# Kernel optimization log

Hardware: AMD Instinct MI355X
Metric: run time of the kernel (lower is better)

## Reference

```python
import jax, jax.numpy as jnp
import numpy as np


def setup_inputs() -> dict:
    key = jax.random.key(0)
    k1, k2, k3 = jax.random.split(key, 3)
    B, L, D, C = 4, 4096, 1024, 1
    x = jax.random.normal(k1, (B, L, D), dtype=jnp.float32)
    kernel = jax.random.normal(k2, (C, D, L), dtype=jnp.float32)
    Dskip = jax.random.normal(k3, (C, D), dtype=jnp.float32)
    return {"x": x, "kernel": kernel, "D": Dskip}


def reference(x, kernel, D):
    # x: [B, L, H]  kernel: [C, H, L]  D: [C, H]
    L = x.shape[1]
    n = 2 * L
    xt = jnp.transpose(x, (0, 2, 1))  # [B, H, L]
    # soft-threshold the kernel: relu(|k| - 0.1) * sign(k)
    k = jax.nn.relu(jnp.abs(kernel) - 0.1) * jnp.sign(kernel)
    k_f = jnp.fft.rfft(k, n=n)          # [C, H, n//2+1] complex
    x_f = jnp.fft.rfft(xt, n=n)         # [B, H, n//2+1] complex
    y_f = jnp.einsum('bhl,chl->bchl', x_f, k_f)
    y = jnp.fft.irfft(y_f, n=n)[..., :L]            # [B, C, H, L]
    y = y + jnp.einsum('bhl,ch->bchl', xt, D)        # skip term
    # rearrange 'b c h l -> b l (c h)'
    Bn, Cn, Hn, Ln = y.shape
    return jnp.transpose(y, (0, 3, 1, 2)).reshape(Bn, Ln, Cn * Hn)
```

## Files before the change

kernel.cpp:

```cpp
#include <hip/hip_runtime.h>


typedef __attribute__((ext_vector_type(8)))  short s16x8;
typedef __attribute__((ext_vector_type(16))) float f32x16;
typedef __attribute__((ext_vector_type(4)))  float f32x4;
typedef __attribute__((ext_vector_type(4)))  unsigned int u32x4;

constexpr int B_ = 4, L_ = 4096, H_ = 1024;
constexpr int PADX = 256;
constexpr int LX = L_ + PADX;
constexpr int LK = L_ + 32;
constexpr int ST = 256;
constexpr int NST = L_ / ST;

constexpr size_t XT_ELEMS = (size_t)B_ * H_ * LX;
constexpr size_t KR_ELEMS = (size_t)2 * H_ * LK;
constexpr size_t OT_ELEMS = (size_t)B_ * H_ * L_;
constexpr size_t WS_NEEDED = (XT_ELEMS + KR_ELEMS + OT_ELEMS) * sizeof(unsigned short);

constexpr int XS_ROW  = 4320;
constexpr int XS_BLKS = XS_ROW / 8;
constexpr int XS_US   = B_ * XS_ROW;
constexpr int KS_US   = 2 * LK;
constexpr int OAREA_DW = 4 * 132;
constexpr int SMEM_BYTES = XS_US * 2 + KS_US * 2 + 4 * OAREA_DW * 4;

constexpr int nHt = H_ / 64, nLt = L_ / 64;
constexpr int NXB = B_ * nLt * nHt;

__device__ __forceinline__ unsigned short f2bf(float f) {
    unsigned int u = __builtin_bit_cast(unsigned int, f);
    u += 0x7fffu + ((u >> 16) & 1u);
    return (unsigned short)(u >> 16);
}
__device__ __forceinline__ float bf2f(unsigned short u) {
    return __builtin_bit_cast(float, (unsigned int)u << 16);
}

__global__ __launch_bounds__(256)
void prep(const float* __restrict__ x, const float* __restrict__ kin,
          const float* __restrict__ Dk,
          unsigned short* __restrict__ xT, unsigned short* __restrict__ kR)
{
    const int bid = blockIdx.x;
    if (bid < NXB) {
        __shared__ float tile[64][65];
        const int b  = bid / (nLt * nHt);
        const int r0 = bid % (nLt * nHt);
        const int l0 = (r0 / nHt) * 64;
        const int h0 = (r0 % nHt) * 64;
        const int j  = threadIdx.x;
        const int h4 = j & 15;
        const int rg = j >> 4;
        #pragma unroll
        for (int it = 0; it < 4; ++it) {
            const int lr = rg + 16 * it;
            const f32x4 v = *(const f32x4*)(x + ((size_t)b * L_ + l0 + lr) * H_ + h0 + 4 * h4);
            tile[lr][4 * h4 + 0] = v.x; tile[lr][4 * h4 + 1] = v.y;
            tile[lr][4 * h4 + 2] = v.z; tile[lr][4 * h4 + 3] = v.w;
        }
        __syncthreads();
        const int lg = j & 7;
        #pragma unroll
        for (int pp = 0; pp < 2; ++pp) {
            const int hh = (j >> 3) + 32 * pp;
            unsigned int w0 = (unsigned int)f2bf(tile[8*lg+0][hh]) | ((unsigned int)f2bf(tile[8*lg+1][hh]) << 16);
            unsigned int w1 = (unsigned int)f2bf(tile[8*lg+2][hh]) | ((unsigned int)f2bf(tile[8*lg+3][hh]) << 16);
            unsigned int w2 = (unsigned int)f2bf(tile[8*lg+4][hh]) | ((unsigned int)f2bf(tile[8*lg+5][hh]) << 16);
            unsigned int w3 = (unsigned int)f2bf(tile[8*lg+6][hh]) | ((unsigned int)f2bf(tile[8*lg+7][hh]) << 16);
            const u32x4 v = {w0, w1, w2, w3};
            *(u32x4*)(xT + ((size_t)b * H_ + h0 + hh) * LX + PADX + l0 + 8 * lg) = v;
        }
        if (l0 == 0) {
            #pragma unroll
            for (int it = 0; it < 8; ++it) {
                const int idx = j + 256 * it;
                const int row = idx >> 5, off = idx & 31;
                const u32x4 z = {};
                *(u32x4*)(xT + ((size_t)b * H_ + h0 + row) * LX + off * 8) = z;
            }
        }
    } else {
        const int h = bid - NXB;
        const float Dv = Dk[h];
        for (int l = (int)threadIdx.x; l < L_; l += 256) {
            const float a = kin[(size_t)h * L_ + l];
            float v = copysignf(fmaxf(fabsf(a) - 0.1f, 0.0f), a);
            if (l == 0) v += Dv;
            const unsigned short bv = f2bf(v);
            kR[(size_t)h * LK + (L_ - 1 - l)] = bv;
            if (l <= L_ - 2)
                kR[((size_t)H_ + h) * LK + (L_ - 2 - l)] = bv;
        }
        if (threadIdx.x < 32) kR[(size_t)h * LK + L_ + threadIdx.x] = 0;
        if (threadIdx.x < 33) kR[((size_t)H_ + h) * LK + (L_ - 1) + threadIdx.x] = 0;
    }
}

#define BODY(DO0, DO1, DO2, DO3)                                            \
  {                                                                         \
    _Pragma("unroll")                                                       \
    for (int i = 0; i < 16; ++i) {                                          \
      u32x4 aw;                                                             \
      aw.x = abase[8*i+0]; aw.y = abase[8*i+1];                             \
      aw.z = abase[8*i+2]; aw.w = abase[8*i+3];                             \
      const s16x8 af = __builtin_bit_cast(s16x8, aw);                       \
      const int io = 32 * (i >> 1);                                         \
      if (DO3) acc3 = __builtin_amdgcn_mfma_f32_32x32x16_bf16(              \
            af, *(const s16x8*)(((i & 1) ? t3b : t3a) + io), acc3, 0,0,0);  \
      if (DO2) acc2 = __builtin_amdgcn_mfma_f32_32x32x16_bf16(              \
            af, *(const s16x8*)(((i & 1) ? t2b : t2a) + io), acc2, 0,0,0);  \
      if (DO1) acc1 = __builtin_amdgcn_mfma_f32_32x32x16_bf16(              \
            af, *(const s16x8*)(((i & 1) ? t1b : t1a) + io), acc1, 0,0,0);  \
      if (DO0) acc0 = __builtin_amdgcn_mfma_f32_32x32x16_bf16(              \
            af, *(const s16x8*)(((i & 1) ? t0b : t0a) + io), acc0, 0,0,0);  \
    }                                                                       \
    abase -= 128;                                                           \
    if (DO3) { t3a -= 256; t3b -= 256; }                                    \
    if (DO2) { t2a -= 256; t2b -= 256; }                                    \
    if (DO1) { t1a -= 256; t1b -= 256; }                                    \
    if (DO0) { t0a -= 256; t0b -= 256; }                                    \
  }

__global__ __launch_bounds__(256, 2)
void longconv_main(const unsigned short* __restrict__ xT,
                   const unsigned short* __restrict__ kR,
                   unsigned int* __restrict__ outT)
{
    __shared__ __align__(16) unsigned char smem[SMEM_BYTES];
    unsigned short* xs = (unsigned short*)smem;
    unsigned short* ks = (unsigned short*)(smem + (size_t)XS_US * 2);
    float* oarea = (float*)(smem + (size_t)XS_US * 2 + (size_t)KS_US * 2);

    const int h   = blockIdx.x;
    const int tid = threadIdx.x;

    constexpr int NXU = XS_BLKS * 4;
    constexpr int NKU = 2 * (LK / 8);
    for (int u = tid; u < NXU + NKU; u += 256) {
        if (u < NXU) {
            const int b = u / XS_BLKS, n = u - b * XS_BLKS;
            const u32x4 v = *(const u32x4*)(xT + ((size_t)b * H_ + h) * LX + 32 + n * 8);
            *(u32x4*)(xs + (size_t)b * XS_ROW + (size_t)(n ^ b) * 8) = v;
        } else {
            const int v2 = u - NXU;
            const int p = v2 / (LK / 8), i = v2 - p * (LK / 8);
            const u32x4 v = *(const u32x4*)(kR + ((size_t)p * H_ + h) * LK + i * 8);
            *(u32x4*)(ks + (size_t)p * LK + (size_t)i * 8) = v;
        }
    }
    __syncthreads();

    const int w  = tid >> 6, ln = tid & 63;
    const int m  = ln & 31,  q  = ln >> 5;
    const int t  = m >> 2,   b  = m & 3;
    const int si0 = w, si1 = 7 - w, si2 = 8 + w, si3 = 15 - w;

    const int base = 3871 - m + 8 * q;
    const int p    = base & 1;
    const unsigned int* abase = (const unsigned int*)(ks + p * LK + (base - p));
    const unsigned short* xrow = xs + (size_t)b * XS_ROW;
    const int nb = 4 * t + q;

    auto mk = [&](int si, int par) -> const unsigned short* {
        const int n = 32 * si + nb + 2 * par;
        return xrow + (size_t)((n ^ b) * 8);
    };
    const unsigned short *t0a = mk(si0, 0), *t0b = mk(si0, 1);
    const unsigned short *t1a = mk(si1, 0), *t1b = mk(si1, 1);
    const unsigned short *t2a = mk(si2, 0), *t2b = mk(si2, 1);
    const unsigned short *t3a = mk(si3, 0), *t3b = mk(si3, 1);

    f32x16 acc0 = {}, acc1 = {}, acc2 = {}, acc3 = {};
    int beta = 0;
    for (; beta <= si0; ++beta) BODY(1, 1, 1, 1);
    for (; beta <= si1; ++beta) BODY(0, 1, 1, 1);
    for (; beta <= si2; ++beta) BODY(0, 0, 1, 1);
    for (; beta <= si3; ++beta) BODY(0, 0, 0, 1);

    float* ar = oarea + w * OAREA_DW;
    auto writeout = [&](const f32x16& acc, int si) {
        const int Ls = si * ST;
        #pragma unroll
        for (int rh = 0; rh < 2; ++rh) {
            #pragma unroll
            for (int rr2 = 0; rr2 < 2; ++rr2) {
                const int base4 = (8 * rr2 + 4 * q + 4 * t) & 15;
                f32x4 qd;
                qd.x = acc[4 * (2 * rh + rr2) + 0];
                qd.y = acc[4 * (2 * rh + rr2) + 1];
                qd.z = acc[4 * (2 * rh + rr2) + 2];
                qd.w = acc[4 * (2 * rh + rr2) + 3];
                *(f32x4*)(ar + b * 132 + 16 * t + base4) = qd;
            }
            __asm__ volatile("s_waitcnt lgkmcnt(0)" ::: "memory");
            #pragma unroll
            for (int bb = 0; bb < 4; ++bb) {
                const int g  = ln >> 3;
                const int uu = (2 * ln) & 15;
                const int s  = (uu + 4 * g) & 15;
                const float v0 = ar[bb * 132 + 16 * g + s];
                const float v1 = ar[bb * 132 + 16 * g + s + 1];
                const int l = 32 * g + 16 * rh + uu;
                const unsigned int pk =
                    (unsigned int)f2bf(v0) | ((unsigned int)f2bf(v1) << 16);
                outT[(((size_t)bb * H_ + h) * L_ + Ls + l) >> 1] = pk;
            }
            __asm__ volatile("s_waitcnt lgkmcnt(0)" ::: "memory");
        }
    };
    writeout(acc0, si0);
    writeout(acc1, si1);
    writeout(acc2, si2);
    writeout(acc3, si3);
}

__global__ __launch_bounds__(256)
void untranspose(const unsigned short* __restrict__ outT, float* __restrict__ out)
{
    __shared__ float tile[64][65];
    const int bid = blockIdx.x;
    const int b  = bid / (nLt * nHt);
    const int r0 = bid % (nLt * nHt);
    const int l0 = (r0 / nHt) * 64;
    const int h0 = (r0 % nHt) * 64;
    const int j  = threadIdx.x;
    const int lg = j & 7;
    #pragma unroll
    for (int pp = 0; pp < 2; ++pp) {
        const int hh = (j >> 3) + 32 * pp;
        const u32x4 v = *(const u32x4*)(outT + ((size_t)b * H_ + h0 + hh) * L_ + l0 + 8 * lg);
        const unsigned short* pu = (const unsigned short*)&v;
        #pragma unroll
        for (int i = 0; i < 8; ++i) tile[8 * lg + i][hh] = bf2f(pu[i]);
    }
    __syncthreads();
    const int hg = j & 15;
    #pragma unroll
    for (int pp = 0; pp < 4; ++pp) {
        const int ll = (j >> 4) + 16 * pp;
        f32x4 v;
        v.x = tile[ll][4 * hg + 0];
        v.y = tile[ll][4 * hg + 1];
        v.z = tile[ll][4 * hg + 2];
        v.w = tile[ll][4 * hg + 3];
        *(f32x4*)(out + ((size_t)b * L_ + l0 + ll) * H_ + h0 + 4 * hg) = v;
    }
}

constexpr int TLf = 32, Uf = 8, Wf = TLf + Uf - 1, HTf = 256;

__global__ __launch_bounds__(HTf)
void longconv_fp32(const float* __restrict__ x, const float* __restrict__ k,
                   const float* __restrict__ Dskip, float* __restrict__ out)
{
    const int h  = blockIdx.y * HTf + threadIdx.x;
    const int b  = blockIdx.z;
    const int lt = (int)gridDim.x - 1 - (int)blockIdx.x;
    const int L0 = lt * TLf;
    const float* __restrict__ xb = x + ((size_t)b * L_) * H_ + h;
    const float* __restrict__ kh = k + (size_t)h * L_;
    float acc[TLf]; float win[Wf];
    #pragma unroll
    for (int i = 0; i < Wf; ++i) {
        const int idx = L0 - (Uf - 1) + i;
        win[i] = (idx >= 0) ? xb[(size_t)idx * H_] : 0.0f;
    }
    const float Dv = Dskip[h];
    #pragma unroll
    for (int jj = 0; jj < TLf; ++jj) acc[jj] = win[jj + Uf - 1] * Dv;
    const int cmax = L0 / Uf + (TLf / Uf) - 1;
    for (int c = 0; c <= cmax; ++c) {
        float kr[Uf];
        #pragma unroll
        for (int u = 0; u < Uf; ++u) {
            const float a = kh[c * Uf + u];
            kr[u] = copysignf(fmaxf(fabsf(a) - 0.1f, 0.0f), a);
        }
        #pragma unroll
        for (int u = 0; u < Uf; ++u)
            #pragma unroll
            for (int jj = 0; jj < TLf; ++jj)
                acc[jj] = fmaf(kr[u], win[jj + (Uf - 1) - u], acc[jj]);
        if (c < cmax) {
            #pragma unroll
            for (int i = Wf - 1; i >= Uf; --i) win[i] = win[i - Uf];
            #pragma unroll
            for (int i = 0; i < Uf; ++i) {
                const int idx = L0 - (c + 1) * Uf - (Uf - 1) + i;
                win[i] = (idx >= 0) ? xb[(size_t)idx * H_] : 0.0f;
            }
        }
    }
    float* __restrict__ ob = out + ((size_t)b * L_ + L0) * H_ + h;
    #pragma unroll
    for (int jj = 0; jj < TLf; ++jj) ob[(size_t)jj * H_] = acc[jj];
}

extern "C" void kernel_launch(void* const* d_in, const int* in_sizes, int n_in,
                              void* d_out, int out_size, void* d_ws, size_t ws_size,
                              hipStream_t stream)
{
    const float* x  = (const float*)d_in[0];
    const float* k  = (const float*)d_in[1];
    const float* Dk = (const float*)d_in[2];
    float* out = (float*)d_out;

    if (ws_size >= WS_NEEDED) {
        unsigned short* xT = (unsigned short*)d_ws;
        unsigned short* kR = xT + XT_ELEMS;
        unsigned short* oT = kR + KR_ELEMS;
        prep<<<dim3(NXB + H_), dim3(256), 0, stream>>>(x, k, Dk, xT, kR);
        longconv_main<<<dim3(H_), dim3(256), 0, stream>>>(xT, kR, (unsigned int*)oT);
        untranspose<<<dim3(NXB), dim3(256), 0, stream>>>(oT, out);
    } else {
        dim3 grid(L_ / TLf, H_ / HTf, B_);
        longconv_fp32<<<grid, dim3(HTf), 0, stream>>>(x, k, Dk, out);
    }
}
```

Baseline: 215.2 us.

## Pair adjacent output strips and reuse B fragments in registers across beta steps

Each wave now handles two pairs of adjacent 256-sample output strips (2w,2w+1 and 14-2w,15-2w) instead of four scattered strips. The x fragment loaded for the lower strip at step beta is exactly what the higher strip needs at step beta+1. It is kept in a 16-entry register array, which roughly halves LDS reads of B fragments. The cost is 32 extra s16x8 registers per thread, which may cause spills or lower occupancy under launch_bounds(256,2).

Result: no change. 211.6 us (-1.7%).

```diff
diff --git a/kernel.cpp b/kernel.cpp
--- a/kernel.cpp
+++ b/kernel.cpp
@@ -97,29 +97,33 @@
     }
 }
 
-#define BODY(DO0, DO1, DO2, DO3)                                            \
-  {                                                                         \
-    _Pragma("unroll")                                                       \
-    for (int i = 0; i < 16; ++i) {                                          \
-      u32x4 aw;                                                             \
-      aw.x = abase[8*i+0]; aw.y = abase[8*i+1];                             \
-      aw.z = abase[8*i+2]; aw.w = abase[8*i+3];                             \
-      const s16x8 af = __builtin_bit_cast(s16x8, aw);                       \
-      const int io = 32 * (i >> 1);                                         \
-      if (DO3) acc3 = __builtin_amdgcn_mfma_f32_32x32x16_bf16(              \
-            af, *(const s16x8*)(((i & 1) ? t3b : t3a) + io), acc3, 0,0,0);  \
-      if (DO2) acc2 = __builtin_amdgcn_mfma_f32_32x32x16_bf16(              \
-            af, *(const s16x8*)(((i & 1) ? t2b : t2a) + io), acc2, 0,0,0);  \
-      if (DO1) acc1 = __builtin_amdgcn_mfma_f32_32x32x16_bf16(              \
-            af, *(const s16x8*)(((i & 1) ? t1b : t1a) + io), acc1, 0,0,0);  \
-      if (DO0) acc0 = __builtin_amdgcn_mfma_f32_32x32x16_bf16(              \
-            af, *(const s16x8*)(((i & 1) ? t0b : t0a) + io), acc0, 0,0,0);  \
-    }                                                                       \
-    abase -= 128;                                                           \
-    if (DO3) { t3a -= 256; t3b -= 256; }                                    \
-    if (DO2) { t2a -= 256; t2b -= 256; }                                    \
-    if (DO1) { t1a -= 256; t1b -= 256; }                                    \
-    if (DO0) { t0a -= 256; t0b -= 256; }                                    \
+#define BODY2(M1, M2)                                                        \
+  {                                                                          \
+    _Pragma("unroll")                                                        \
+    for (int i = 0; i < 16; ++i) {                                           \
+      u32x4 aw;                                                              \
+      aw.x = abase[8*i+0]; aw.y = abase[8*i+1];                              \
+      aw.z = abase[8*i+2]; aw.w = abase[8*i+3];                              \
+      const s16x8 af = __builtin_bit_cast(s16x8, aw);                        \
+      const int io = 32 * (i >> 1);                                          \
+      if (M2 >= 1) accH2 = __builtin_amdgcn_mfma_f32_32x32x16_bf16(          \
+            af, held2[i], accH2, 0, 0, 0);                                   \
+      if (M2 == 2) {                                                         \
+        const s16x8 nf = *(const s16x8*)(((i & 1) ? p2b : p2a) + io);        \
+        accL2 = __builtin_amdgcn_mfma_f32_32x32x16_bf16(af, nf, accL2,0,0,0);\
+        held2[i] = nf;                                                       \
+      }                                                                      \
+      if (M1 >= 1) accH1 = __builtin_amdgcn_mfma_f32_32x32x16_bf16(          \
+            af, held1[i], accH1, 0, 0, 0);                                   \
+      if (M1 == 2) {                                                         \
+        const s16x8 nf = *(const s16x8*)(((i & 1) ? p1b : p1a) + io);        \
+        accL1 = __builtin_amdgcn_mfma_f32_32x32x16_bf16(af, nf, accL1,0,0,0);\
+        held1[i] = nf;                                                       \
+      }                                                                      \
+    }                                                                        \
+    abase -= 128;                                                            \
+    if (M1 == 2) { p1a -= 256; p1b -= 256; }                                 \
+    if (M2 == 2) { p2a -= 256; p2b -= 256; }                                 \
   }
 
 __global__ __launch_bounds__(256, 2)
@@ -154,7 +158,8 @@
     const int w  = tid >> 6, ln = tid & 63;
     const int m  = ln & 31,  q  = ln >> 5;
     const int t  = m >> 2,   b  = m & 3;
-    const int si0 = w, si1 = 7 - w, si2 = 8 + w, si3 = 15 - w;
+    const int s1 = 2 * w;
+    const int s2 = 14 - 2 * w;
 
     const int base = 3871 - m + 8 * q;
     const int p    = base & 1;
@@ -166,17 +171,24 @@
         const int n = 32 * si + nb + 2 * par;
         return xrow + (size_t)((n ^ b) * 8);
     };
-    const unsigned short *t0a = mk(si0, 0), *t0b = mk(si0, 1);
-    const unsigned short *t1a = mk(si1, 0), *t1b = mk(si1, 1);
-    const unsigned short *t2a = mk(si2, 0), *t2b = mk(si2, 1);
-    const unsigned short *t3a = mk(si3, 0), *t3b = mk(si3, 1);
-
-    f32x16 acc0 = {}, acc1 = {}, acc2 = {}, acc3 = {};
-    int beta = 0;
-    for (; beta <= si0; ++beta) BODY(1, 1, 1, 1);
-    for (; beta <= si1; ++beta) BODY(0, 1, 1, 1);
-    for (; beta <= si2; ++beta) BODY(0, 0, 1, 1);
-    for (; beta <= si3; ++beta) BODY(0, 0, 0, 1);
+    const unsigned short *p1a = mk(s1 + 1, 0), *p1b = mk(s1 + 1, 1);
+    const unsigned short *p2a = mk(s2 + 1, 0), *p2b = mk(s2 + 1, 1);
+
+    s16x8 held1[16], held2[16];
+    #pragma unroll
+    for (int i = 0; i < 16; ++i) {
+        const int io = 32 * (i >> 1);
+        held1[i] = *(const s16x8*)(((i & 1) ? p1b : p1a) + io);
+        held2[i] = *(const s16x8*)(((i & 1) ? p2b : p2a) + io);
+    }
+    p1a -= 256; p1b -= 256; p2a -= 256; p2b -= 256;
+
+    f32x16 accL1 = {}, accH1 = {}, accL2 = {}, accH2 = {};
+
+    for (int beta = 0; beta <= s1; ++beta) BODY2(2, 2);
+    BODY2(1, 2);
+    for (int beta = s1 + 2; beta <= s2; ++beta) BODY2(0, 2);
+    BODY2(0, 1);
 
     float* ar = oarea + w * OAREA_DW;
     auto writeout = [&](const f32x16& acc, int si) {
@@ -209,10 +221,10 @@
             __asm__ volatile("s_waitcnt lgkmcnt(0)" ::: "memory");
         }
     };
-    writeout(acc0, si0);
-    writeout(acc1, si1);
-    writeout(acc2, si2);
-    writeout(acc3, si3);
+    writeout(accL1, s1);
+    writeout(accH1, s1 + 1);
+    writeout(accL2, s2);
+    writeout(accH2, s2 + 1);
 }
 
 __global__ __launch_bounds__(256)
```
